# Performance work log

Hardware: AMD Instinct MI355X
Metric: run time of the kernel (lower is better)

## Reference

```python
import jax, jax.numpy as jnp
import numpy as np

N = 100000       # nodes
E0 = 1600000     # edges without self loops
E = E0 + N       # with self loops appended (attr 0), matching add_self_loops
DIN = 128        # input_dim
HID = 64         # nb_hidden_gnn (per-head out_channels)
HEADS = 4
EMB = 128
L = 3            # nb_layer
NEG_SLOPE = 0.2
BN_EPS = 1e-5


def setup_inputs() -> dict:
    key = jax.random.key(0)
    ks = jax.random.split(key, 12)
    # edges with no self loops; self loops (i,i) appended with edge_attr 0
    row = jax.random.randint(ks[0], (E0,), 0, N)
    off = jax.random.randint(ks[1], (E0,), 1, N)
    col = (row + off) % N
    loops = jnp.arange(N, dtype=row.dtype)
    edge_index = jnp.stack([jnp.concatenate([row, loops]),
                            jnp.concatenate([col, loops])])
    edge_attr = jnp.concatenate([jax.random.normal(ks[2], (E0, 1), jnp.float32),
                                 jnp.zeros((N, 1), jnp.float32)])
    x = jax.random.normal(ks[3], (N, DIN), jnp.float32)
    HC = HEADS * HID
    linN0 = jax.random.normal(ks[4], (DIN, HC)) * HC ** -0.5
    linN_rest = jax.random.normal(ks[5], (L - 1, HID, HC)) * HC ** -0.5
    linE_all = jax.random.normal(ks[6], (L, 1, HEADS)) * HEADS ** -0.5  # nb_edge_attr=1
    att_all = jax.random.normal(ks[7], (L, HEADS, 2 * HID + 1)) * (2 * HID + 1) ** -0.5
    bias_all = jnp.zeros((L, HID))  # concat=False -> bias [out_channels]
    bn_gamma = jnp.ones((L - 1, HID))
    bn_beta = jnp.zeros((L - 1, HID))
    W = jax.random.normal(ks[8], (HID, EMB)) * HID ** -0.5
    b = jnp.zeros((EMB,))
    return {"x": x, "edge_index": edge_index, "edge_attr": edge_attr,
            "linN0": linN0, "linN_rest": linN_rest, "linE_all": linE_all,
            "att_all": att_all, "bias_all": bias_all,
            "bn_gamma": bn_gamma, "bn_beta": bn_beta, "W": W, "b": b}


def _gcn_layer(x, row, col, edge_attr, linN, linE, att, bias, bn):
    n = x.shape[0]
    if bn is not None:
        gamma, beta = bn
        mu = x.mean(axis=0)
        var = x.var(axis=0)
        x = (x - mu) * jax.lax.rsqrt(var + BN_EPS) * gamma + beta
    h = (x @ linN).reshape(n, HEADS, HID)                 # [N,H,C]
    e = (edge_attr @ linE)                                # [E,H] (nb_edge_attr=1)
    att_i = att[:, :HID]                                  # [H,C]
    att_j = att[:, HID:2 * HID]                           # [H,C]
    att_e = att[:, 2 * HID:]                              # [H,1]
    # per-node partial scores avoid gathering full features twice
    s_i = jnp.einsum('nhc,hc->nh', h, att_i)
    s_j = jnp.einsum('nhc,hc->nh', h, att_j)
    logits = s_i[row] + s_j[col] + e * att_e[:, 0]        # [E,H]
    logits = jax.nn.leaky_relu(logits, NEG_SLOPE)
    # segment softmax over destination nodes (edge_index[1])
    m = jax.ops.segment_max(logits, col, num_segments=n)
    p = jnp.exp(logits - m[col])
    denom = jax.ops.segment_sum(p, col, num_segments=n)
    alpha = p / (denom[col] + 1e-16)
    # message: alpha * x[source], scatter-add to destination
    msg = alpha[:, :, None] * h[row]                      # [E,H,C]
    out = jax.ops.segment_sum(msg, col, num_segments=n)   # [N,H,C]
    out = out.mean(axis=1) + bias + h.mean(axis=1)        # concat=False, res=True
    return jax.nn.relu(out)


def reference(x, edge_index, edge_attr, linN0, linN_rest, linE_all, att_all,
              bias_all, bn_gamma, bn_beta, W, b):
    row, col = edge_index[0], edge_index[1]
    emb = x
    for l in range(L):
        linN = linN0 if l == 0 else linN_rest[l - 1]
        bn = None if l == 0 else (bn_gamma[l - 1], bn_beta[l - 1])
        emb = _gcn_layer(emb, row, col, edge_attr, linN, linE_all[l],
                         att_all[l], bias_all[l], bn)
    return emb @ W + b
```

## Files before the change

### kernel.cpp

```cpp
#include <hip/hip_runtime.h>
#include <math.h>

#define NN 100000
#define E0E 1600000
#define EE (E0E + NN)
#define NEG 0.2f
#define BNEPS 1e-5f
#define LOG2E 1.4426950408889634f

typedef float f4 __attribute__((ext_vector_type(4)));
typedef float f2 __attribute__((ext_vector_type(2)));
typedef short s8v __attribute__((ext_vector_type(8)));

__device__ __forceinline__ float wred_max(float v) {
#pragma unroll
  for (int m = 1; m < 64; m <<= 1) v = fmaxf(v, __shfl_xor(v, m, 64));
  return v;
}
__device__ __forceinline__ float wred_sum(float v) {
#pragma unroll
  for (int m = 1; m < 64; m <<= 1) v += __shfl_xor(v, m, 64);
  return v;
}
__device__ __forceinline__ float sel4(float a0, float a1, float a2, float a3, int hd) {
  return (hd & 2) ? ((hd & 1) ? a3 : a2) : ((hd & 1) ? a1 : a0);
}
__device__ __forceinline__ unsigned short f2bf(float x) {
  unsigned u = __float_as_uint(x);
  return (unsigned short)((u + 0x7fffu + ((u >> 16) & 1u)) >> 16);
}
__device__ __forceinline__ float bf2f(unsigned short s) {
  return __uint_as_float(((unsigned)s) << 16);
}

__global__ void k_init(int* cnt, double* bnsum, int n) {
  int i = blockIdx.x * blockDim.x + threadIdx.x;
  if (i < n) cnt[i] = 0;
  if (i < 256) bnsum[i] = 0.0;
}
__global__ void k_count(const int* __restrict__ col, int* cnt, int e) {
  int i = blockIdx.x * blockDim.x + threadIdx.x;
  if (i < e) atomicAdd(&cnt[col[i]], 1);
}
#define SCAN_T 1024
__global__ void k_scan1(const int* __restrict__ cnt, int* partial, int n, int chunk) {
  int i = blockIdx.x * blockDim.x + threadIdx.x;
  int beg = i * chunk, end = min(n, beg + chunk);
  int s = 0;
  for (int j = beg; j < end; ++j) s += cnt[j];
  partial[i] = s;
}
__global__ void k_scan2(int* partial) {
  __shared__ int lds[SCAN_T];
  int t = threadIdx.x;
  int v = partial[t];
  lds[t] = v;
  __syncthreads();
  for (int off = 1; off < SCAN_T; off <<= 1) {
    int add = (t >= off) ? lds[t - off] : 0;
    __syncthreads();
    lds[t] += add;
    __syncthreads();
  }
  partial[t] = lds[t] - v;
}
__global__ void k_scan3(const int* __restrict__ cnt, const int* __restrict__ partial,
                        int* rowptr, int* cursor, int n, int chunk, int etot) {
  int i = blockIdx.x * blockDim.x + threadIdx.x;
  int beg = i * chunk, end = min(n, beg + chunk);
  int run = partial[i];
  for (int j = beg; j < end; ++j) {
    rowptr[j] = run;
    cursor[j] = run;
    run += cnt[j];
  }
  if (i == SCAN_T - 1) rowptr[n] = etot;
}
__global__ void k_scatter(const int* __restrict__ row, const int* __restrict__ col,
                          const float* __restrict__ ea, int* cursor, int2* csr, int e) {
  int i = blockIdx.x * blockDim.x + threadIdx.x;
  if (i < e) {
    int c = col[i];
    int p = atomicAdd(&cursor[c], 1);
    csr[p] = make_int2(row[i], __float_as_int(ea[i]));
  }
}

__global__ void k_bnstats(const unsigned short* __restrict__ x, double* sums, int n) {
  int f = threadIdx.x & 63;
  int rt = (blockIdx.x * blockDim.x + threadIdx.x) >> 6;
  int rstride = (gridDim.x * blockDim.x) >> 6;
  double s = 0.0, q = 0.0;
  for (int r = rt; r < n; r += rstride) {
    double v = (double)bf2f(x[(size_t)r * 64 + f]);
    s += v;
    q += v * v;
  }
  __shared__ double ls[256], lq[256];
  ls[threadIdx.x] = s;
  lq[threadIdx.x] = q;
  __syncthreads();
  if (threadIdx.x < 64) {
    s = ls[threadIdx.x] + ls[threadIdx.x + 64] + ls[threadIdx.x + 128] + ls[threadIdx.x + 192];
    q = lq[threadIdx.x] + lq[threadIdx.x + 64] + lq[threadIdx.x + 128] + lq[threadIdx.x + 192];
    atomicAdd(&sums[f], s);
    atomicAdd(&sums[64 + f], q);
  }
}

__global__ void k_prepw(const float* __restrict__ W, const double* __restrict__ bnsum,
                        const float* __restrict__ gamma, const float* __restrict__ beta,
                        const float* __restrict__ bin, unsigned short* __restrict__ Wt,
                        float* __restrict__ cvec, int K, int N, int mode) {
  __shared__ float ABl[128];
  __shared__ float cred[4][64];
  int t = threadIdx.x;
  if (mode == 1) {
    if (t < 64) {
      double mean = bnsum[t] / NN;
      double var = bnsum[64 + t] / NN - mean * mean;
      float A = gamma[t] * rsqrtf((float)var + BNEPS);
      ABl[t] = A;
      ABl[64 + t] = beta[t] - (float)mean * A;
    }
    __syncthreads();
  }
  int cl = t & 63, kq = t >> 6;
  int col = blockIdx.x * 64 + cl;
  int kn = K >> 2;
  int k0 = kq * kn;
  float c = 0.f;
#pragma unroll 8
  for (int k = k0; k < k0 + kn; ++k) {
    float w = W[k * N + col];
    float a = 1.f, b = 0.f;
    if (mode == 1) { a = ABl[k]; b = ABl[64 + k]; }
    Wt[col * K + k] = f2bf(a * w);
    c = fmaf(b, w, c);
  }
  cred[kq][cl] = c;
  __syncthreads();
  if (kq == 0) {
    float cc = cred[0][cl] + cred[1][cl] + cred[2][cl] + cred[3][cl];
    if (mode == 2) cc += bin[col];
    cvec[col] = cc;
  }
}

template <int K, int CT, bool ATT, bool OB, bool INBF>
__global__ __launch_bounds__(256, 2) void k_gemm(const void* __restrict__ xv,
                                                 const unsigned short* __restrict__ Wt,
                                                 const float* __restrict__ cvec,
                                                 const float* __restrict__ att,
                                                 void* __restrict__ houtv,
                                                 float* __restrict__ s_i,
                                                 float* __restrict__ s_j, int n,
                                                 int ntiles) {
  constexpr int KS = K / 32;
  constexpr int ROWB = 2 * K;
  constexpr int CPR = K / 8;
  constexpr int NCOL = 4 * CT * 16;
  __shared__ unsigned char xs[64 * ROWB];
  const int lane = threadIdx.x & 63;
  const int wv = threadIdx.x >> 6;
  const int l15 = lane & 15;
  const int lq = lane >> 4;
  const int colbase = wv * CT * 16;

  s8v wfr[CT][KS];
#pragma unroll
  for (int ct = 0; ct < CT; ++ct)
#pragma unroll
    for (int ks = 0; ks < KS; ++ks)
      wfr[ct][ks] = *(const s8v*)&Wt[(size_t)(colbase + ct * 16 + l15) * K + ks * 32 + lq * 8];
  float cb[CT][4];
#pragma unroll
  for (int ct = 0; ct < CT; ++ct)
#pragma unroll
    for (int r = 0; r < 4; ++r) cb[ct][r] = cvec[colbase + ct * 16 + lq * 4 + r];
  float ati[ATT ? CT : 1][4], atj[ATT ? CT : 1][4];
  if constexpr (ATT) {
    const float* ar = att + wv * 129;
#pragma unroll
    for (int ct = 0; ct < CT; ++ct)
#pragma unroll
      for (int r = 0; r < 4; ++r) {
        int cc = ct * 16 + lq * 4 + r;
        ati[ct][r] = ar[cc];
        atj[ct][r] = ar[64 + cc];
      }
  }

  for (int t = blockIdx.x; t < ntiles; t += gridDim.x) {
    const int row0 = t * 64;
    __syncthreads();
#pragma unroll
    for (int i = 0; i < (64 * CPR) / 256; ++i) {
      int c = threadIdx.x + i * 256;
      int row = c / CPR, kc = c % CPR;
      int rg = min(row0 + row, n - 1);
      int dst = row * ROWB + ((kc * 16) ^ ((row & 7) << 4));
      if constexpr (INBF) {
        const unsigned short* xin = (const unsigned short*)xv;
        *(s8v*)&xs[dst] = *(const s8v*)&xin[(size_t)rg * K + kc * 8];
      } else {
        const float* xin = (const float*)xv;
        const float* xp = xin + (size_t)rg * K + kc * 8;
        f4 a0 = *(const f4*)xp;
        f4 a1 = *(const f4*)(xp + 4);
        union { s8v v; unsigned short u[8]; } pk;
        pk.u[0] = f2bf(a0[0]); pk.u[1] = f2bf(a0[1]); pk.u[2] = f2bf(a0[2]); pk.u[3] = f2bf(a0[3]);
        pk.u[4] = f2bf(a1[0]); pk.u[5] = f2bf(a1[1]); pk.u[6] = f2bf(a1[2]); pk.u[7] = f2bf(a1[3]);
        *(s8v*)&xs[dst] = pk.v;
      }
    }
    __syncthreads();
    f4 acc[4][CT];
#pragma unroll
    for (int rt = 0; rt < 4; ++rt)
#pragma unroll
      for (int ct = 0; ct < CT; ++ct) acc[rt][ct] = (f4)0.f;
#pragma unroll
    for (int ks = 0; ks < KS; ++ks) {
      s8v xf[4];
#pragma unroll
      for (int rt = 0; rt < 4; ++rt) {
        int row = rt * 16 + l15;
        int kb = ks * 64 + lq * 16;
        xf[rt] = *(const s8v*)&xs[row * ROWB + (kb ^ ((row & 7) << 4))];
      }
#pragma unroll
      for (int rt = 0; rt < 4; ++rt)
#pragma unroll
        for (int ct = 0; ct < CT; ++ct)
          acc[rt][ct] = __builtin_amdgcn_mfma_f32_16x16x32_bf16(wfr[ct][ks], xf[rt],
                                                                acc[rt][ct], 0, 0, 0);
    }
#pragma unroll
    for (int rt = 0; rt < 4; ++rt) {
      if (row0 + rt * 16 >= n) continue;
      const size_t xrow = (size_t)(row0 + rt * 16 + l15);
      float v[CT][4];
#pragma unroll
      for (int ct = 0; ct < CT; ++ct)
#pragma unroll
        for (int r = 0; r < 4; ++r) v[ct][r] = acc[rt][ct][r] + cb[ct][r];
      if constexpr (OB) {
        float* outp = (float*)houtv;
#pragma unroll
        for (int ct = 0; ct < CT; ++ct) {
          f4 o;
          o[0] = v[ct][0]; o[1] = v[ct][1]; o[2] = v[ct][2]; o[3] = v[ct][3];
          *(f4*)&outp[xrow * NCOL + colbase + ct * 16 + lq * 4] = o;
        }
      } else {
        unsigned short* hout = (unsigned short*)houtv;
#pragma unroll
        for (int ct = 0; ct < CT; ++ct) {
          ushort4 hb4;
          hb4.x = f2bf(v[ct][0]); hb4.y = f2bf(v[ct][1]);
          hb4.z = f2bf(v[ct][2]); hb4.w = f2bf(v[ct][3]);
          *(ushort4*)&hout[xrow * NCOL + colbase + ct * 16 + lq * 4] = hb4;
        }
      }
      if constexpr (ATT) {
        float pi = 0.f, pj = 0.f;
#pragma unroll
        for (int ct = 0; ct < CT; ++ct)
#pragma unroll
          for (int r = 0; r < 4; ++r) {
            pi = fmaf(v[ct][r], ati[ct][r], pi);
            pj = fmaf(v[ct][r], atj[ct][r], pj);
          }
        pi += __shfl_xor(pi, 16, 64); pi += __shfl_xor(pi, 32, 64);
        pj += __shfl_xor(pj, 16, 64); pj += __shfl_xor(pj, 32, 64);
        if (lane < 16) {
          s_i[xrow * 4 + wv] = pi;
          s_j[xrow * 4 + wv] = pj;
        }
      }
    }
  }
}

__global__ __launch_bounds__(256) void k_edge(const int* __restrict__ rowptr,
                                              const int2* __restrict__ csr,
                                              const float* __restrict__ s_i,
                                              const float* __restrict__ s_j,
                                              const unsigned short* __restrict__ hb,
                                              const float* __restrict__ linE,
                                              const float* __restrict__ att,
                                              const float* __restrict__ bias,
                                              unsigned short* __restrict__ xout, int n) {
  __shared__ float lp[4][64][4];
  __shared__ int lsrc[4][64];
  const unsigned char* hb8 = (const unsigned char*)hb;
  const int lane = threadIdx.x & 63;
  const int wid = threadIdx.x >> 6;
  const int lane8 = lane * 8;
  int v = blockIdx.x * 4 + wid;
  if (v >= n) return;
  v = __builtin_amdgcn_readfirstlane(v);
  const int base = rowptr[v];
  const int deg = rowptr[v + 1] - base;

  const float coef0 = linE[0] * att[0 * 129 + 128];
  const float coef1 = linE[1] * att[1 * 129 + 128];
  const float coef2 = linE[2] * att[2 * 129 + 128];
  const float coef3 = linE[3] * att[3 * 129 + 128];
  const float sj0 = s_j[(size_t)v * 4 + 0];
  const float sj1 = s_j[(size_t)v * 4 + 1];
  const float sj2 = s_j[(size_t)v * 4 + 2];
  const float sj3 = s_j[(size_t)v * 4 + 3];

  auto edge_logits = [&](int i, int& src, float& g0, float& g1, float& g2, float& g3) {
    int2 pk = csr[i];
    src = pk.x;
    float ea = __int_as_float(pk.y);
    f4 siv = *(const f4*)&s_i[(size_t)src * 4];
    g0 = siv[0] + sj0 + ea * coef0; g0 = fmaxf(g0, g0 * NEG);
    g1 = siv[1] + sj1 + ea * coef1; g1 = fmaxf(g1, g1 * NEG);
    g2 = siv[2] + sj2 + ea * coef2; g2 = fmaxf(g2, g2 * NEG);
    g3 = siv[3] + sj3 + ea * coef3; g3 = fmaxf(g3, g3 * NEG);
  };

  const int hd = lane >> 4;
  f4 acc;
  {
    ushort4 hr = *(const ushort4*)(hb8 + ((unsigned)v << 9) + lane8);
    acc[0] = bf2f(hr.x); acc[1] = bf2f(hr.y); acc[2] = bf2f(hr.z); acc[3] = bf2f(hr.w);
  }

  bool fast = (deg <= 64);
  if (fast) {
    float g0 = -INFINITY, g1 = -INFINITY, g2 = -INFINITY, g3 = -INFINITY;
    int src = 0;
    bool valid = lane < deg;
    if (valid) edge_logits(base + lane, src, g0, g1, g2, g3);
    float m0 = wred_max(g0), m1 = wred_max(g1), m2 = wred_max(g2), m3 = wred_max(g3);
    float p0 = valid ? exp2f((g0 - m0) * LOG2E) : 0.f;
    float p1 = valid ? exp2f((g1 - m1) * LOG2E) : 0.f;
    float p2 = valid ? exp2f((g2 - m2) * LOG2E) : 0.f;
    float p3 = valid ? exp2f((g3 - m3) * LOG2E) : 0.f;
    float d0 = wred_sum(p0), d1 = wred_sum(p1), d2 = wred_sum(p2), d3 = wred_sum(p3);
    float rd0 = 1.f / (d0 + 1e-16f);
    float rd1 = 1.f / (d1 + 1e-16f);
    float rd2 = 1.f / (d2 + 1e-16f);
    float rd3 = 1.f / (d3 + 1e-16f);
    if (valid) {
      f4 pp;
      pp[0] = p0 * rd0; pp[1] = p1 * rd1; pp[2] = p2 * rd2; pp[3] = p3 * rd3;
      *(f4*)&lp[wid][lane][0] = pp;
      lsrc[wid][lane] = src << 9;
    }
    for (int e = 0; e < deg; ++e) {
      int off = lsrc[wid][e];
      float a = lp[wid][e][hd];
      ushort4 h0 = *(const ushort4*)(hb8 + (unsigned)(off + lane8));
      acc[0] = fmaf(a, bf2f(h0.x), acc[0]);
      acc[1] = fmaf(a, bf2f(h0.y), acc[1]);
      acc[2] = fmaf(a, bf2f(h0.z), acc[2]);
      acc[3] = fmaf(a, bf2f(h0.w), acc[3]);
    }
  } else {
    float m0 = -INFINITY, m1 = -INFINITY, m2 = -INFINITY, m3 = -INFINITY;
    for (int c0 = 0; c0 < deg; c0 += 64) {
      int i = c0 + lane;
      if (i < deg) {
        int src; float g0, g1, g2, g3;
        edge_logits(base + i, src, g0, g1, g2, g3);
        m0 = fmaxf(m0, g0); m1 = fmaxf(m1, g1); m2 = fmaxf(m2, g2); m3 = fmaxf(m3, g3);
      }
    }
    m0 = wred_max(m0); m1 = wred_max(m1); m2 = wred_max(m2); m3 = wred_max(m3);
    float d0 = 0, d1 = 0, d2 = 0, d3 = 0;
    for (int c0 = 0; c0 < deg; c0 += 64) {
      int i = c0 + lane;
      if (i < deg) {
        int src; float g0, g1, g2, g3;
        edge_logits(base + i, src, g0, g1, g2, g3);
        d0 += exp2f((g0 - m0) * LOG2E);
        d1 += exp2f((g1 - m1) * LOG2E);
        d2 += exp2f((g2 - m2) * LOG2E);
        d3 += exp2f((g3 - m3) * LOG2E);
      }
    }
    d0 = wred_sum(d0); d1 = wred_sum(d1); d2 = wred_sum(d2); d3 = wred_sum(d3);
    float msel = sel4(m0, m1, m2, m3, hd);
    float rdsel = 1.f / (sel4(d0, d1, d2, d3, hd) + 1e-16f);
    const float sjsel = sel4(sj0, sj1, sj2, sj3, hd);
    const float cfsel = sel4(coef0, coef1, coef2, coef3, hd);
    for (int e = base; e < base + deg; ++e) {
      int2 pk = csr[e];
      int src = pk.x;
      float ea = __int_as_float(pk.y);
      f4 siv = *(const f4*)&s_i[(size_t)src * 4];
      float lg = sel4(siv[0], siv[1], siv[2], siv[3], hd) + sjsel + ea * cfsel;
      lg = fmaxf(lg, lg * NEG);
      float a = exp2f((lg - msel) * LOG2E) * rdsel;
      ushort4 hr = *(const ushort4*)(hb8 + ((unsigned)src << 9) + lane8);
      acc[0] = fmaf(a, bf2f(hr.x), acc[0]);
      acc[1] = fmaf(a, bf2f(hr.y), acc[1]);
      acc[2] = fmaf(a, bf2f(hr.z), acc[2]);
      acc[3] = fmaf(a, bf2f(hr.w), acc[3]);
    }
  }
#pragma unroll
  for (int m = 16; m < 64; m <<= 1) {
    acc[0] += __shfl_xor(acc[0], m, 64);
    acc[1] += __shfl_xor(acc[1], m, 64);
    acc[2] += __shfl_xor(acc[2], m, 64);
    acc[3] += __shfl_xor(acc[3], m, 64);
  }
  if (lane < 16) {
    f4 bv = *(const f4*)&bias[lane * 4];
    ushort4 o;
    o.x = f2bf(fmaxf(acc[0] * 0.25f + bv[0], 0.f));
    o.y = f2bf(fmaxf(acc[1] * 0.25f + bv[1], 0.f));
    o.z = f2bf(fmaxf(acc[2] * 0.25f + bv[2], 0.f));
    o.w = f2bf(fmaxf(acc[3] * 0.25f + bv[3], 0.f));
    *(ushort4*)&xout[(size_t)v * 64 + lane * 4] = o;
  }
}

extern "C" void kernel_launch(void* const* d_in, const int* in_sizes, int n_in,
                              void* d_out, int out_size, void* d_ws, size_t ws_size,
                              hipStream_t stream) {
  const float* x_in = (const float*)d_in[0];
  const int* ei = (const int*)d_in[1];
  const float* eattr = (const float*)d_in[2];
  const float* linN0 = (const float*)d_in[3];
  const float* linNr = (const float*)d_in[4];
  const float* linE = (const float*)d_in[5];
  const float* attA = (const float*)d_in[6];
  const float* biasA = (const float*)d_in[7];
  const float* bng = (const float*)d_in[8];
  const float* bnb = (const float*)d_in[9];
  const float* W = (const float*)d_in[10];
  const float* bb = (const float*)d_in[11];
  float* out = (float*)d_out;

  const int* row = ei;
  const int* col = ei + EE;

  char* ws = (char*)d_ws;
  size_t o = 0;
  auto alloc = [&](size_t bytes) {
    void* p = ws + o;
    o += (bytes + 255) & ~(size_t)255;
    return p;
  };
  int* cnt = (int*)alloc((size_t)NN * 4);
  int* cursor = (int*)alloc((size_t)NN * 4);
  int* rowptr = (int*)alloc((size_t)(NN + 1) * 4);
  int* partial = (int*)alloc((size_t)SCAN_T * 4);
  int2* csr = (int2*)alloc((size_t)EE * 8);
  unsigned short* h = (unsigned short*)alloc((size_t)NN * 256 * 2);
  float* si = (float*)alloc((size_t)NN * 4 * 4);
  float* sj = (float*)alloc((size_t)NN * 4 * 4);
  unsigned short* xa = (unsigned short*)alloc((size_t)NN * 64 * 2);
  unsigned short* xb = (unsigned short*)alloc((size_t)NN * 64 * 2);
  double* bnsum = (double*)alloc(256 * 8);
  unsigned short* Wt = (unsigned short*)alloc((size_t)256 * 128 * 2);
  float* cvec = (float*)alloc(256 * 4);
  if (o > ws_size) return;

  const int chunk = (NN + SCAN_T - 1) / SCAN_T;
  const int NTILES = (NN + 63) / 64;
  const int GG = 391;

  k_init<<<(NN + 255) / 256, 256, 0, stream>>>(cnt, bnsum, NN);
  k_count<<<(EE + 255) / 256, 256, 0, stream>>>(col, cnt, EE);
  k_scan1<<<4, 256, 0, stream>>>(cnt, partial, NN, chunk);
  k_scan2<<<1, SCAN_T, 0, stream>>>(partial);
  k_scan3<<<4, 256, 0, stream>>>(cnt, partial, rowptr, cursor, NN, chunk, EE);
  k_scatter<<<(EE + 255) / 256, 256, 0, stream>>>(row, col, eattr, cursor, csr, EE);

  k_prepw<<<4, 256, 0, stream>>>(linN0, nullptr, nullptr, nullptr, nullptr, Wt, cvec, 128, 256, 0);
  k_gemm<128, 4, true, false, false><<<GG, 256, 0, stream>>>(x_in, Wt, cvec, attA + 0, h, si, sj,
                                                             NN, NTILES);
  k_edge<<<NN / 4, 256, 0, stream>>>(rowptr, csr, si, sj, h, linE + 0, attA + 0, biasA + 0,
                                     xa, NN);

  k_bnstats<<<256, 256, 0, stream>>>(xa, bnsum, NN);
  k_prepw<<<4, 256, 0, stream>>>(linNr, bnsum, bng, bnb, nullptr, Wt, cvec, 64, 256, 1);
  k_gemm<64, 4, true, false, true><<<GG, 256, 0, stream>>>(xa, Wt, cvec, attA + 516, h, si, sj,
                                                           NN, NTILES);
  k_edge<<<NN / 4, 256, 0, stream>>>(rowptr, csr, si, sj, h, linE + 4, attA + 516, biasA + 64,
                                     xb, NN);

  k_bnstats<<<256, 256, 0, stream>>>(xb, bnsum + 128, NN);
  k_prepw<<<4, 256, 0, stream>>>(linNr + 64 * 256, bnsum + 128, bng + 64, bnb + 64, nullptr,
                                 Wt, cvec, 64, 256, 1);
  k_gemm<64, 4, true, false, true><<<GG, 256, 0, stream>>>(xb, Wt, cvec, attA + 2 * 516, h, si, sj,
                                                           NN, NTILES);
  k_edge<<<NN / 4, 256, 0, stream>>>(rowptr, csr, si, sj, h, linE + 8, attA + 2 * 516,
                                     biasA + 128, xa, NN);

  k_prepw<<<2, 256, 0, stream>>>(W, nullptr, nullptr, nullptr, bb, Wt, cvec, 64, 128, 2);
  k_gemm<64, 2, false, true, true><<<GG, 256, 0, stream>>>(xa, Wt, cvec, nullptr, out, nullptr,
                                                           nullptr, NN, NTILES);
}
```

Baseline: 835.7 us.

## Fuse final linear projection into last edge kernel and merge scan kernels

The three-kernel prefix scan becomes a single-block kernel that computes chunk sums, scans them in LDS and writes rowptr and cursor. The last k_edge instantiation now keeps its bf16 output in LDS and multiplies it by the final 64x128 weight matrix staged in LDS, writing the fp32 output directly. This removes the final GEMM launch and the write and re-read of the intermediate embedding. The cost is extra LDS use and a per-block weight load in the last edge kernel, which may lower occupancy.

```diff
diff --git a/kernel.cpp b/kernel.cpp
--- a/kernel.cpp
+++ b/kernel.cpp
@@ -43,18 +43,14 @@
   if (i < e) atomicAdd(&cnt[col[i]], 1);
 }
 #define SCAN_T 1024
-__global__ void k_scan1(const int* __restrict__ cnt, int* partial, int n, int chunk) {
-  int i = blockIdx.x * blockDim.x + threadIdx.x;
-  int beg = i * chunk, end = min(n, beg + chunk);
+__global__ void k_scanF(const int* __restrict__ cnt, int* rowptr, int* cursor,
+                        int n, int chunk, int etot) {
+  __shared__ int lds[SCAN_T];
+  int t = threadIdx.x;
+  int beg = t * chunk, end = min(n, beg + chunk);
   int s = 0;
   for (int j = beg; j < end; ++j) s += cnt[j];
-  partial[i] = s;
-}
-__global__ void k_scan2(int* partial) {
-  __shared__ int lds[SCAN_T];
-  int t = threadIdx.x;
-  int v = partial[t];
-  lds[t] = v;
+  lds[t] = s;
   __syncthreads();
   for (int off = 1; off < SCAN_T; off <<= 1) {
     int add = (t >= off) ? lds[t - off] : 0;
@@ -62,19 +58,13 @@
     lds[t] += add;
     __syncthreads();
   }
-  partial[t] = lds[t] - v;
-}
-__global__ void k_scan3(const int* __restrict__ cnt, const int* __restrict__ partial,
-                        int* rowptr, int* cursor, int n, int chunk, int etot) {
-  int i = blockIdx.x * blockDim.x + threadIdx.x;
-  int beg = i * chunk, end = min(n, beg + chunk);
-  int run = partial[i];
+  int run = lds[t] - s;
   for (int j = beg; j < end; ++j) {
     rowptr[j] = run;
     cursor[j] = run;
     run += cnt[j];
   }
-  if (i == SCAN_T - 1) rowptr[n] = etot;
+  if (t == SCAN_T - 1) rowptr[n] = etot;
 }
 __global__ void k_scatter(const int* __restrict__ row, const int* __restrict__ col,
                           const float* __restrict__ ea, int* cursor, int2* csr, int e) {
@@ -283,6 +273,7 @@
   }
 }
 
+template <bool FUSE>
 __global__ __launch_bounds__(256) void k_edge(const int* __restrict__ rowptr,
                                               const int2* __restrict__ csr,
                                               const float* __restrict__ s_i,
@@ -291,15 +282,28 @@
                                               const float* __restrict__ linE,
                                               const float* __restrict__ att,
                                               const float* __restrict__ bias,
-                                              unsigned short* __restrict__ xout, int n) {
+                                              unsigned short* __restrict__ xout,
+                                              const unsigned short* __restrict__ Wfin,
+                                              const float* __restrict__ bb,
+                                              float* __restrict__ outF, int n) {
   __shared__ float lp[4][64][4];
   __shared__ int lsrc[4][64];
+  __shared__ unsigned short obuf[4][64];
+  extern __shared__ unsigned short wlds[];
   const unsigned char* hb8 = (const unsigned char*)hb;
   const int lane = threadIdx.x & 63;
   const int wid = threadIdx.x >> 6;
   const int lane8 = lane * 8;
+
+  if constexpr (FUSE) {
+    for (int idx = threadIdx.x; idx < 128 * 16; idx += 256) {
+      int c = idx >> 4, ch = idx & 15;
+      *(ushort4*)&wlds[c * 68 + ch * 4] = *(const ushort4*)&Wfin[c * 64 + ch * 4];
+    }
+    __syncthreads();
+  }
+
   int v = blockIdx.x * 4 + wid;
-  if (v >= n) return;
   v = __builtin_amdgcn_readfirstlane(v);
   const int base = rowptr[v];
   const int deg = rowptr[v + 1] - base;
@@ -419,7 +423,30 @@
     o.y = f2bf(fmaxf(acc[1] * 0.25f + bv[1], 0.f));
     o.z = f2bf(fmaxf(acc[2] * 0.25f + bv[2], 0.f));
     o.w = f2bf(fmaxf(acc[3] * 0.25f + bv[3], 0.f));
-    *(ushort4*)&xout[(size_t)v * 64 + lane * 4] = o;
+    if constexpr (FUSE) {
+      *(ushort4*)&obuf[wid][lane * 4] = o;
+    } else {
+      *(ushort4*)&xout[(size_t)v * 64 + lane * 4] = o;
+    }
+  }
+  if constexpr (FUSE) {
+    float t0 = 0.f, t1 = 0.f;
+#pragma unroll
+    for (int ch = 0; ch < 8; ++ch) {
+      union { s8v v; unsigned short u[8]; } ou;
+      ou.v = *(const s8v*)&obuf[wid][ch * 8];
+      union { s8v v; unsigned short u[8]; } wa, wb;
+      wa.v = *(const s8v*)&wlds[lane * 68 + ch * 8];
+      wb.v = *(const s8v*)&wlds[(lane + 64) * 68 + ch * 8];
+#pragma unroll
+      for (int j = 0; j < 8; ++j) {
+        float oj = bf2f(ou.u[j]);
+        t0 = fmaf(oj, bf2f(wa.u[j]), t0);
+        t1 = fmaf(oj, bf2f(wb.u[j]), t1);
+      }
+    }
+    outF[(size_t)v * 128 + lane] = t0 + bb[lane];
+    outF[(size_t)v * 128 + 64 + lane] = t1 + bb[64 + lane];
   }
 }
 
@@ -453,7 +480,6 @@
   int* cnt = (int*)alloc((size_t)NN * 4);
   int* cursor = (int*)alloc((size_t)NN * 4);
   int* rowptr = (int*)alloc((size_t)(NN + 1) * 4);
-  int* partial = (int*)alloc((size_t)SCAN_T * 4);
   int2* csr = (int2*)alloc((size_t)EE * 8);
   unsigned short* h = (unsigned short*)alloc((size_t)NN * 256 * 2);
   float* si = (float*)alloc((size_t)NN * 4 * 4);
@@ -462,7 +488,9 @@
   unsigned short* xb = (unsigned short*)alloc((size_t)NN * 64 * 2);
   double* bnsum = (double*)alloc(256 * 8);
   unsigned short* Wt = (unsigned short*)alloc((size_t)256 * 128 * 2);
+  unsigned short* Wt2 = (unsigned short*)alloc((size_t)128 * 64 * 2);
   float* cvec = (float*)alloc(256 * 4);
+  float* cvec2 = (float*)alloc(256 * 4);
   if (o > ws_size) return;
 
   const int chunk = (NN + SCAN_T - 1) / SCAN_T;
@@ -471,33 +499,29 @@
 
   k_init<<<(NN + 255) / 256, 256, 0, stream>>>(cnt, bnsum, NN);
   k_count<<<(EE + 255) / 256, 256, 0, stream>>>(col, cnt, EE);
-  k_scan1<<<4, 256, 0, stream>>>(cnt, partial, NN, chunk);
-  k_scan2<<<1, SCAN_T, 0, stream>>>(partial);
-  k_scan3<<<4, 256, 0, stream>>>(cnt, partial, rowptr, cursor, NN, chunk, EE);
+  k_scanF<<<1, SCAN_T, 0, stream>>>(cnt, rowptr, cursor, NN, chunk, EE);
   k_scatter<<<(EE + 255) / 256, 256, 0, stream>>>(row, col, eattr, cursor, csr, EE);
+  k_prepw<<<2, 256, 0, stream>>>(W, nullptr, nullptr, nullptr, nullptr, Wt2, cvec2, 64, 128, 0);
 
   k_prepw<<<4, 256, 0, stream>>>(linN0, nullptr, nullptr, nullptr, nullptr, Wt, cvec, 128, 256, 0);
-  k_gemm<128, 4, true, false, false><<<GG, 256, 0, stream>>>(x_in, Wt, cvec, attA + 0, h, si, sj,
-                                                             NN, NTILES);
-  k_edge<<<NN / 4, 256, 0, stream>>>(rowptr, csr, si, sj, h, linE + 0, attA + 0, biasA + 0,
-                                     xa, NN);
+  k_gemm<128, 4, true, false, false><<<GG, 256, 0, stream>>>(x_in, Wt, cvec, attA + 0,
+                                                             h, si, sj, NN, NTILES);
+  k_edge<false><<<NN / 4, 256, 0, stream>>>(rowptr, csr, si, sj, h, linE + 0, attA + 0,
+                                            biasA + 0, xa, nullptr, nullptr, nullptr, NN);
 
   k_bnstats<<<256, 256, 0, stream>>>(xa, bnsum, NN);
   k_prepw<<<4, 256, 0, stream>>>(linNr, bnsum, bng, bnb, nullptr, Wt, cvec, 64, 256, 1);
-  k_gemm<64, 4, true, false, true><<<GG, 256, 0, stream>>>(xa, Wt, cvec, attA + 516, h, si, sj,
-                                                           NN, NTILES);
-  k_edge<<<NN / 4, 256, 0, stream>>>(rowptr, csr, si, sj, h, linE + 4, attA + 516, biasA + 64,
-                                     xb, NN);
+  k_gemm<64, 4, true, false, true><<<GG, 256, 0, stream>>>(xa, Wt, cvec, attA + 516,
+                                                           h, si, sj, NN, NTILES);
+  k_edge<false><<<NN / 4, 256, 0, stream>>>(rowptr, csr, si, sj, h, linE + 4, attA + 516,
+                                            biasA + 64, xb, nullptr, nullptr, nullptr, NN);
 
   k_bnstats<<<256, 256, 0, stream>>>(xb, bnsum + 128, NN);
   k_prepw<<<4, 256, 0, stream>>>(linNr + 64 * 256, bnsum + 128, bng + 64, bnb + 64, nullptr,
                                  Wt, cvec, 64, 256, 1);
-  k_gemm<64, 4, true, false, true><<<GG, 256, 0, stream>>>(xb, Wt, cvec, attA + 2 * 516, h, si, sj,
-                                                           NN, NTILES);
-  k_edge<<<NN / 4, 256, 0, stream>>>(rowptr, csr, si, sj, h, linE + 8, attA + 2 * 516,
-                                     biasA + 128, xa, NN);
-
-  k_prepw<<<2, 256, 0, stream>>>(W, nullptr, nullptr, nullptr, bb, Wt, cvec, 64, 128, 2);
-  k_gemm<64, 2, false, true, true><<<GG, 256, 0, stream>>>(xa, Wt, cvec, nullptr, out, nullptr,
-                                                           nullptr, NN, NTILES);
-}
+  k_gemm<64, 4, true, false, true><<<GG, 256, 0, stream>>>(xb, Wt, cvec, attA + 2 * 516,
+                                                           h, si, sj, NN, NTILES);
+  k_edge<true><<<NN / 4, 256, 128 * 68 * 2, stream>>>(rowptr, csr, si, sj, h, linE + 8,
+                                                      attA + 2 * 516, biasA + 128, nullptr,
+                                                      Wt2, bb, out, NN);
+}
```

Result: slower. 1.117 ms (+33.7%).
